# Kernel tuning notes

Hardware: AMD Instinct MI355X
Metric: run time of the kernel (lower is better)

## Reference

```python
import jax, jax.numpy as jnp
import numpy as np

B, S, D_MODEL, H = 2, 2048, 2048, 16
DQK = D_MODEL // H            # 128
DV = D_MODEL * 2 // H // 3    # 85 (GLU branch)
SCALE = DQK ** -0.5
ROPE_BASE = 10000.0


def apply_rope(x):
    # x: [B, S, H, D], NeoX-style half rotation
    D = x.shape[-1]
    half = D // 2
    inv_freq = 1.0 / (ROPE_BASE ** (jnp.arange(half, dtype=jnp.float32) / half))
    ang = jnp.arange(x.shape[1], dtype=jnp.float32)[:, None] * inv_freq[None, :]  # [S, half]
    cos = jnp.cos(ang)[None, :, None, :]
    sin = jnp.sin(ang)[None, :, None, :]
    x1, x2 = x[..., :half], x[..., half:]
    return jnp.concatenate([x1 * cos - x2 * sin, x2 * cos + x1 * sin], axis=-1)


def setup_inputs() -> dict:
    key = jax.random.key(0)
    ks = jax.random.split(key, 12)
    init = lambda k, shape, fan_in: jax.random.uniform(k, shape, jnp.float32, -1.0, 1.0) * (fan_in ** -0.5)
    q = jax.random.normal(ks[0], (B, S, D_MODEL), jnp.float32)
    k = jax.random.normal(ks[1], (B, S, D_MODEL), jnp.float32)
    v = jax.random.normal(ks[2], (B, S, D_MODEL), jnp.float32)
    # causal boolean mask: True = masked (upper triangle)
    mask = jnp.triu(jnp.ones((S, S), dtype=bool), k=1)
    Wq = init(ks[3], (D_MODEL, DQK * H), D_MODEL)
    bq = init(ks[4], (DQK * H,), D_MODEL)
    Wk = init(ks[5], (D_MODEL, DQK * H), D_MODEL)
    bk = init(ks[6], (DQK * H,), D_MODEL)
    Wv = init(ks[7], (D_MODEL, DV * H * 2), D_MODEL)
    bv = init(ks[8], (DV * H * 2,), D_MODEL)
    Wo = init(ks[9], (DV * H, D_MODEL), DV * H)
    bo = init(ks[10], (D_MODEL,), DV * H)
    return {"q": q, "k": k, "v": v, "mask": mask,
            "Wq": Wq, "bq": bq, "Wk": Wk, "bk": bk,
            "Wv": Wv, "bv": bv, "Wo": Wo, "bo": bo}


def reference(q, k, v, mask, Wq, bq, Wk, bk, Wv, bv, Wo, bo):
    qp = q @ Wq + bq                      # [B,S,H*DQK]
    kp = k @ Wk + bk                      # [B,S,H*DQK]
    vp = v @ Wv + bv                      # [B,S,2*H*DV]
    # GLU over the FULL last dim (matches torch chunk(2, dim=-1) before unflatten)
    half = DV * H
    vg = vp[..., :half] * jax.nn.silu(vp[..., half:])   # [B,S,H*DV]
    qh = qp.reshape(B, S, H, DQK)
    kh = kp.reshape(B, S, H, DQK)
    vh = vg.reshape(B, S, H, DV)
    qh = apply_rope(qh)
    kh = apply_rope(kh)
    # [B,H,S,D]
    qh = qh.transpose(0, 2, 1, 3)
    kh = kh.transpose(0, 2, 1, 3)
    vh = vh.transpose(0, 2, 1, 3)
    score = jnp.einsum('bhqd,bhkd->bhqk', qh, kh) * SCALE  # [B,H,S,S]
    score = jnp.where(mask[None, None, :, :], -jnp.inf, score)
    attn = jax.nn.softmax(score, axis=-1)
    o = jnp.einsum('bhqk,bhkd->bhqd', attn, vh)            # [B,H,S,DV]
    o = o.transpose(0, 2, 1, 3).reshape(B, S, H * DV)
    return o @ Wo + bo                                     # [B,S,D_MODEL]
```

## Files before the change

### kernel.cpp

```cpp
#include <hip/hip_runtime.h>
#include <cstdint>
#include <cmath>

typedef __bf16 bf16;
typedef __bf16 bf16x8 __attribute__((ext_vector_type(8)));
typedef float f32x4 __attribute__((ext_vector_type(4)));

#define B_      2
#define S_      2048
#define H_      16
#define DQK_    128
#define DV_     85
#define DVP_    96
#define DMODEL_ 2048
#define NKV_    1360
#define KH_     1536
#define NV_     2720
#define NVP_    2816
#define SCALE_  0.08838834764831845f
#define QSCALE_ 0.12752044442215615f
#define M2_     16.0f
#define L2_10K_ 13.287712379549449f

__device__ __forceinline__ void lds_cp16(const void* g, void* l) {
    __builtin_amdgcn_global_load_lds(
        (const __attribute__((address_space(1))) unsigned int*)(uintptr_t)g,
        (__attribute__((address_space(3))) unsigned int*)(uintptr_t)l,
        16, 0, 0);
}

__global__ __launch_bounds__(256) void detect_dtype(const unsigned int* __restrict__ w,
                                                    int* __restrict__ flag) {
    __shared__ int cnt;
    if (threadIdx.x == 0) cnt = 0;
    __syncthreads();
    unsigned v = w[threadIdx.x];
    unsigned e = (v >> 7) & 0xFFu;
    if (e > 100u && e < 140u) atomicAdd(&cnt, 1);
    __syncthreads();
    if (threadIdx.x == 0) *flag = (cnt >= 200) ? 1 : 0;
}

__global__ __launch_bounds__(256) void norm_mat(const void* __restrict__ src, bf16* __restrict__ dst,
                                                const int* __restrict__ flag, long n8) {
    long i = (long)blockIdx.x * 256 + threadIdx.x;
    if (i >= n8) return;
    if (*flag) {
        ((bf16x8*)dst)[i] = ((const bf16x8*)src)[i];
    } else {
        const float* s = (const float*)src;
        bf16x8 v;
#pragma unroll
        for (int j = 0; j < 8; ++j) v[j] = (bf16)s[i * 8 + j];
        ((bf16x8*)dst)[i] = v;
    }
}

__global__ __launch_bounds__(256) void norm_bias4(
    const void* __restrict__ s0, const void* __restrict__ s1,
    const void* __restrict__ s2, const void* __restrict__ s3,
    float* __restrict__ d0, float* __restrict__ d1,
    float* __restrict__ d2, float* __restrict__ d3,
    const int* __restrict__ flag) {
    int j = blockIdx.x * 256 + threadIdx.x;
    const void* s; float* d;
    if (j < DMODEL_) { s = s0; d = d0; }
    else if ((j -= DMODEL_) < DMODEL_) { s = s1; d = d1; }
    else if ((j -= DMODEL_) < NV_) { s = s2; d = d2; }
    else if ((j -= NV_) < DMODEL_) { s = s3; d = d3; }
    else return;
    d[j] = (*flag) ? (float)((const bf16*)s)[j] : ((const float*)s)[j];
}

__global__ __launch_bounds__(256) void transpose_qk_dyn(
    const void* __restrict__ inq, const void* __restrict__ ink,
    bf16* __restrict__ outq, bf16* __restrict__ outk, const int* __restrict__ flag) {
    __shared__ bf16 tile[32][33];
    const bool isbf = (*flag != 0);
    const void* in = blockIdx.z ? ink : inq;
    bf16* out = blockIdx.z ? outk : outq;
    int r0 = blockIdx.x * 32, c0 = blockIdx.y * 32;
    int tx = threadIdx.x, ty = threadIdx.y;
#pragma unroll
    for (int i = 0; i < 32; i += 8) {
        size_t idx = (size_t)(r0 + ty + i) * DMODEL_ + c0 + tx;
        tile[ty + i][tx] = isbf ? ((const bf16*)in)[idx] : (bf16)((const float*)in)[idx];
    }
    __syncthreads();
#pragma unroll
    for (int i = 0; i < 32; i += 8)
        out[(size_t)(c0 + ty + i) * DMODEL_ + r0 + tx] = tile[tx][ty + i];
}

__global__ __launch_bounds__(256) void transpose_wvi_dyn(
    const void* __restrict__ in, bf16* __restrict__ out, const int* __restrict__ flag) {
    __shared__ bf16 tile[32][34];
    const bool isbf = (*flag != 0);
    int n0 = blockIdx.x * 32, k0 = blockIdx.y * 32;
    int tx = threadIdx.x, ty = threadIdx.y;
    int fl = (n0 >> 1) + (tx & 15), vg = tx >> 4;
    int c = vg * NKV_ + fl;
    int nl = 2 * (tx & 15) + vg;
#pragma unroll
    for (int i = 0; i < 32; i += 8) {
        bf16 v = (bf16)0.0f;
        if (fl < NKV_) {
            size_t idx = (size_t)(k0 + ty + i) * NV_ + c;
            v = isbf ? ((const bf16*)in)[idx] : (bf16)((const float*)in)[idx];
        }
        tile[ty + i][nl] = v;
    }
    __syncthreads();
#pragma unroll
    for (int i = 0; i < 32; i += 8)
        out[(size_t)(n0 + ty + i) * DMODEL_ + k0 + tx] = tile[tx][ty + i];
}

__global__ __launch_bounds__(256) void transpose_wo_dyn(
    const void* __restrict__ in, bf16* __restrict__ out, const int* __restrict__ flag) {
    __shared__ bf16 tile[32][33];
    const bool isbf = (*flag != 0);
    int k0 = blockIdx.x * 32, n0 = blockIdx.y * 32;
    int tx = threadIdx.x, ty = threadIdx.y;
#pragma unroll
    for (int i = 0; i < 32; i += 8) {
        int k = k0 + ty + i, c = n0 + tx;
        int hh = k / DVP_, dd = k - hh * DVP_;
        bf16 v = (bf16)0.0f;
        if (dd < DV_) {
            size_t idx = (size_t)(hh * DV_ + dd) * DMODEL_ + c;
            v = isbf ? ((const bf16*)in)[idx] : (bf16)((const float*)in)[idx];
        }
        tile[ty + i][tx] = v;
    }
    __syncthreads();
#pragma unroll
    for (int i = 0; i < 32; i += 8) {
        int n = n0 + ty + i, k = k0 + tx;
        out[(size_t)n * KH_ + k] = tile[tx][ty + i];
    }
}

template <int NT, class AF>
__device__ __forceinline__ void gemm256_loop(
    AF aaddr, const bf16* __restrict__ Bt, int ldb, int n0,
    bf16* sA, bf16* sB, f32x4 (&acc)[8][4])
{
    const int tid = threadIdx.x, lane = tid & 63, w = tid >> 6;
    const int fm = lane & 15, quad = lane >> 4;
    const int wm = (w >> 2) * 128, wn = (w & 3) * 64;
    const int row0 = tid >> 2;
    const int kk8 = (((tid >> 3) ^ tid) & 3) * 8;
    const int qsz = (quad ^ ((fm >> 1) & 3)) * 8;

    auto stageA = [&](int u) {
        const int ri = u & 3, c = u * 32 + kk8;
        lds_cp16(aaddr(row0, c),       &sA[ri * 8192 + w * 512]);
        lds_cp16(aaddr(row0 + 128, c), &sA[ri * 8192 + 4096 + w * 512]);
    };
    auto stageB = [&](int u) {
        const int ri = u & 3, c = u * 32 + kk8;
        lds_cp16(Bt + (size_t)(n0 + row0) * ldb + c,       &sB[ri * 8192 + w * 512]);
        lds_cp16(Bt + (size_t)(n0 + row0 + 128) * ldb + c, &sB[ri * 8192 + 4096 + w * 512]);
    };

    stageA(0); stageB(0); stageA(1); stageB(1);
    asm volatile("s_waitcnt vmcnt(4)" ::: "memory");
    __builtin_amdgcn_sched_barrier(0);
    __builtin_amdgcn_s_barrier();
    __builtin_amdgcn_sched_barrier(0);

    for (int t = 0; t < NT; ++t) {
        const int u0 = 2 * t;
        const bool pre = (t + 1 < NT);
        bf16x8 af[8], bfv[2];
#pragma unroll
        for (int p = 0; p < 4; ++p) {
            const int kh = p >> 1, nh = p & 1;
            const int ri = (u0 + kh) & 3;
            if (nh == 0) {
#pragma unroll
                for (int i = 0; i < 8; ++i)
                    af[i] = *(const bf16x8*)&sA[ri * 8192 + (wm + i * 16 + fm) * 32 + qsz];
            }
#pragma unroll
            for (int j = 0; j < 2; ++j)
                bfv[j] = *(const bf16x8*)&sB[ri * 8192 + (wn + nh * 32 + j * 16 + fm) * 32 + qsz];
            if (pre) {
                if      (p == 0) stageA(u0 + 2);
                else if (p == 1) stageB(u0 + 2);
                else if (p == 2) stageA(u0 + 3);
                else             stageB(u0 + 3);
            }
            __builtin_amdgcn_sched_barrier(0);
            __builtin_amdgcn_s_barrier();
            asm volatile("s_waitcnt lgkmcnt(0)" ::: "memory");
            __builtin_amdgcn_sched_barrier(0);
            __builtin_amdgcn_s_setprio(1);
#pragma unroll
            for (int i = 0; i < 8; ++i)
#pragma unroll
                for (int j = 0; j < 2; ++j)
                    acc[i][nh * 2 + j] = __builtin_amdgcn_mfma_f32_16x16x32_bf16(
                        af[i], bfv[j], acc[i][nh * 2 + j], 0, 0, 0);
            __builtin_amdgcn_s_setprio(0);
            __builtin_amdgcn_sched_barrier(0);
            if (nh == 1) {
                if (pre) asm volatile("s_waitcnt vmcnt(4)" ::: "memory");
                else     asm volatile("s_waitcnt vmcnt(0)" ::: "memory");
                __builtin_amdgcn_sched_barrier(0);
            }
            __builtin_amdgcn_s_barrier();
            __builtin_amdgcn_sched_barrier(0);
        }
    }
}

__global__ __launch_bounds__(512, 2) void gemm_qk_rope256(
    const bf16* __restrict__ Aq, const bf16* __restrict__ Ak,
    const bf16* __restrict__ Btq, const bf16* __restrict__ Btk,
    const float* __restrict__ bq, const float* __restrict__ bk,
    bf16* __restrict__ qt, bf16* __restrict__ ktp) {
    extern __shared__ char smem[];
    bf16* sA = (bf16*)smem;
    bf16* sB = (bf16*)(smem + 65536);
    const int z = blockIdx.z;
    const bf16* A     = z ? Ak  : Aq;
    const bf16* Bt    = z ? Btk : Btq;
    const float* bias = z ? bk  : bq;
    bf16* dst         = z ? ktp : qt;
    const float qs    = z ? 1.0f : QSCALE_;
    const int tid = threadIdx.x, lane = tid & 63, w = tid >> 6;
    const int fm = lane & 15, quad = lane >> 4;
    const int wm = (w >> 2) * 128, wn = (w & 3) * 64;
    const int m0 = blockIdx.x * 256, n0 = blockIdx.y * 256;
    f32x4 acc[8][4] = {};
    auto aaddr = [&](int row, int k) -> const bf16* {
        return A + (size_t)(m0 + row) * DMODEL_ + k;
    };
    gemm256_loop<32>(aaddr, Bt, DMODEL_, n0, sA, sB, acc);

    float bv[4];
#pragma unroll
    for (int jn = 0; jn < 4; ++jn) bv[jn] = bias[n0 + wn + jn * 16 + fm];
    const int b = m0 >> 11, sb = m0 & (S_ - 1);
    const int hbase = n0 >> 7;
    bf16* ep = (bf16*)smem;
    __syncthreads();
#pragma unroll
    for (int g = 0; g < 4; ++g) {
        if ((w >> 2) == (g >> 1)) {
#pragma unroll
            for (int i2 = 0; i2 < 4; ++i2) {
                const int i = (g & 1) * 4 + i2;
#pragma unroll
                for (int jn = 0; jn < 4; ++jn)
#pragma unroll
                    for (int r = 0; r < 4; ++r)
                        ep[(i2 * 16 + quad * 4 + r) * 264 + wn + jn * 16 + fm] =
                            (bf16)(acc[i][jn][r] + bv[jn]);
            }
        }
        __syncthreads();
#pragma unroll
        for (int it2 = 0; it2 < 4; ++it2) {
            int task = it2 * 512 + tid;
            int lr = task >> 5, ch = task & 31;
            int s = sb + g * 64 + lr;
            int h = hbase + (ch >> 4);
            int cl0 = (ch * 8) & 127;
            bf16x8 v  = *(const bf16x8*)&ep[lr * 264 + ch * 8];
            bf16x8 uu = *(const bf16x8*)&ep[lr * 264 + ((ch * 8) ^ 64)];
            bf16x8 o8;
#pragma unroll
            for (int j = 0; j < 8; ++j) {
                int cl = cl0 + j, dd = cl & 63;
                float ang = (float)s * exp2f(-(float)dd * (L2_10K_ / 64.0f));
                float sn, cs;
                __sincosf(ang, &sn, &cs);
                float x = (float)v[j], y = (float)uu[j];
                float ov = (cl < 64) ? (x * cs - y * sn) : (x * cs + y * sn);
                o8[j] = (bf16)(ov * qs);
            }
            *(bf16x8*)&dst[((size_t)(b * H_ + h) * S_ + s) * DQK_ + cl0] = o8;
        }
        __syncthreads();
    }
}

__global__ __launch_bounds__(512, 2) void gemm_v_swiglu256(
    const bf16* __restrict__ A, const bf16* __restrict__ Bt,
    const float* __restrict__ bias, bf16* __restrict__ vt) {
    extern __shared__ char smem[];
    bf16* sA = (bf16*)smem;
    bf16* sB = (bf16*)(smem + 65536);
    const int tid = threadIdx.x, lane = tid & 63, w = tid >> 6;
    const int fm = lane & 15, quad = lane >> 4;
    const int wm = (w >> 2) * 128, wn = (w & 3) * 64;
    const int m0 = blockIdx.x * 256, n0 = blockIdx.y * 256;
    f32x4 acc[8][4] = {};
    auto aaddr = [&](int row, int k) -> const bf16* {
        return A + (size_t)(m0 + row) * DMODEL_ + k;
    };
    gemm256_loop<32>(aaddr, Bt, DMODEL_, n0, sA, sB, acc);

    float bv[4];
#pragma unroll
    for (int jn = 0; jn < 4; ++jn) {
        int col = n0 + wn + jn * 16 + fm;
        bv[jn] = (col < NV_) ? bias[(col & 1) * NKV_ + (col >> 1)] : 0.0f;
    }
    bf16* ep2 = (bf16*)smem;
    __syncthreads();
    const bool isval = ((fm & 1) == 0);
    const int flb = (wn >> 1) + (fm >> 1);
#pragma unroll
    for (int i = 0; i < 8; ++i)
#pragma unroll
        for (int jn = 0; jn < 4; ++jn)
#pragma unroll
            for (int r = 0; r < 4; ++r) {
                float ag = acc[i][jn][r] + bv[jn];
                float part = __shfl_xor(ag, 1, 64);
                if (isval) {
                    float gg = part;
                    float out = ag * gg / (1.0f + __expf(-gg));
                    ep2[(flb + jn * 8) * 264 + wm + i * 16 + quad * 4 + r] = (bf16)out;
                }
            }
    __syncthreads();
    const int b = m0 >> 11, s0 = m0 & (S_ - 1);
#pragma unroll
    for (int it2 = 0; it2 < 8; ++it2) {
        int task = it2 * 512 + tid;
        int fl_local = task >> 5, ch = task & 31;
        int flat = blockIdx.y * 128 + fl_local;
        if (flat < NKV_) {
            int h = (flat * 1543) >> 17;
            int d = flat - h * DV_;
            bf16x8 vv = *(const bf16x8*)&ep2[fl_local * 264 + ch * 8];
            *(bf16x8*)&vt[((size_t)(b * H_ + h) * DVP_ + d) * S_ + s0 + ch * 8] = vv;
        }
    }
}

__global__ __launch_bounds__(256) void vt_pad(bf16* __restrict__ vt) {
    int idx = blockIdx.x * 256 + threadIdx.x;
    if (idx >= 32 * 11 * 2048) return;
    int s = idx & (S_ - 1);
    int rest = idx >> 11;
    int dpad = 85 + rest % 11;
    int bh = rest / 11;
    vt[((size_t)bh * DVP_ + dpad) * S_ + s] = (bf16)((dpad == 95) ? 1.0f : 0.0f);
}

__global__ __launch_bounds__(256) void gemm_bt_oh(
    const bf16* __restrict__ Oh, const bf16* __restrict__ Bt,
    const float* __restrict__ bias, bf16* __restrict__ C, float* __restrict__ Cf,
    const int* __restrict__ outflag) {
    __shared__ bf16 As[128 * 32];
    __shared__ bf16 Bs[128 * 32];
    const int t = threadIdx.x, lane = t & 63, w = t >> 6;
    const int m0 = blockIdx.x * 128, n0 = blockIdx.y * 128;
    const int wm = (w >> 1) * 64, wn = (w & 1) * 64;
    const int fm = lane & 15, quad = lane >> 4, fk = quad * 8;
    const int srow = lane >> 2, scol = (lane & 3) * 8;
    f32x4 acc[4][4] = {};
    for (int k0 = 0; k0 < KH_; k0 += 32) {
        __syncthreads();
#pragma unroll
        for (int j = 0; j < 2; ++j) {
            int c = j * 4 + w;
            int m = m0 + c * 16 + srow;
            int k = k0 + scol;
            int hh = k / DVP_, dd = k - hh * DVP_;
            const bf16* ga = Oh + ((size_t)((m >> 11) * H_ + hh) * S_ + (m & (S_ - 1))) * DVP_ + dd;
            lds_cp16(ga, &As[c * 512]);
            lds_cp16(Bt + (size_t)(n0 + c * 16 + srow) * KH_ + k0 + scol, &Bs[c * 512]);
        }
        __syncthreads();
        bf16x8 af[4], bfr[4];
#pragma unroll
        for (int i = 0; i < 4; ++i) {
            af[i]  = *(const bf16x8*)&As[(wm + i * 16 + fm) * 32 + fk];
            bfr[i] = *(const bf16x8*)&Bs[(wn + i * 16 + fm) * 32 + fk];
        }
#pragma unroll
        for (int i = 0; i < 4; ++i)
#pragma unroll
            for (int jn = 0; jn < 4; ++jn)
                acc[i][jn] = __builtin_amdgcn_mfma_f32_16x16x32_bf16(af[i], bfr[jn], acc[i][jn], 0, 0, 0);
    }
    bool bf16out = (*outflag != 0);
#pragma unroll
    for (int jn = 0; jn < 4; ++jn) {
        int col = n0 + wn + jn * 16 + fm;
        float bv = bias[col];
#pragma unroll
        for (int i = 0; i < 4; ++i) {
            int rowb = m0 + wm + i * 16 + quad * 4;
            if (bf16out) {
#pragma unroll
                for (int r = 0; r < 4; ++r)
                    C[(size_t)(rowb + r) * DMODEL_ + col] = (bf16)(acc[i][jn][r] + bv);
            } else {
#pragma unroll
                for (int r = 0; r < 4; ++r)
                    Cf[(size_t)(rowb + r) * DMODEL_ + col] = acc[i][jn][r] + bv;
            }
        }
    }
}

__global__ __launch_bounds__(256) void attn_split(
    const bf16* __restrict__ qt, const bf16* __restrict__ kt,
    const bf16* __restrict__ vt,
    bf16* __restrict__ Opart, float* __restrict__ lpart) {
    const int bh = blockIdx.x, qb = blockIdx.y, split = blockIdx.z;
    if (split * 8 > qb) return;
    __shared__ bf16 Ks[64 * 128];
    __shared__ bf16 Vs[96 * 64];
    __shared__ bf16 plds[4][16 * 72];
    const int t = threadIdx.x, lane = t & 63, w = t >> 6;
    const int fm = lane & 15, quad = lane >> 4;
    const int h = bh & 15, b = bh >> 4;
    const int q0 = qb * 64 + w * 16;
    const int g = qb >> 3;
    const int pidx = bh * 80 + 4 * g * (g + 1) + (qb & 7) * (g + 1) + split;

    const bf16* qbase = qt + ((size_t)(b * H_ + h) * S_ + q0 + fm) * DQK_ + quad * 8;
    bf16x8 aq[4];
#pragma unroll
    for (int kb = 0; kb < 4; ++kb) aq[kb] = *(const bf16x8*)(qbase + kb * 32);
    const bf16* kbase = kt + (size_t)(b * H_ + h) * S_ * DQK_;
    const bf16* vbase = vt + (size_t)(b * H_ + h) * DVP_ * S_;

    const float NEG_INF = -__builtin_inff();
    f32x4 oacc[6] = {};
    bf16* pl = &plds[w][0];

    const int t0 = split * 8;
    const int t1 = min(t0 + 8, qb + 1);
    for (int it = t0; it < t1; ++it) {
        const int k0 = it * 64;
        __syncthreads();
#pragma unroll
        for (int iw = 0; iw < 4; ++iw) {
            int flat = (w * 4 + iw) * 64 + lane;
            int r = flat >> 4, c = (flat & 15) ^ (r & 15);
            lds_cp16(kbase + (size_t)(k0 + r) * DQK_ + c * 8, &Ks[(w * 4 + iw) * 512]);
        }
#pragma unroll
        for (int iw = 0; iw < 3; ++iw) {
            int flat = (w * 3 + iw) * 64 + lane;
            int r = flat >> 3, c = (flat & 7) ^ (r & 7);
            lds_cp16(vbase + (size_t)r * S_ + k0 + c * 8, &Vs[(w * 3 + iw) * 512]);
        }
        __syncthreads();
        f32x4 sc[4] = {};
#pragma unroll
        for (int nt = 0; nt < 4; ++nt) {
            if (k0 + nt * 16 <= q0 + 15) {
                const int row16 = (nt * 16 + fm) * 16;
#pragma unroll
                for (int kb = 0; kb < 4; ++kb) {
                    const bf16* kp = &Ks[(row16 + ((kb * 4 + quad) ^ fm)) * 8];
                    sc[nt] = __builtin_amdgcn_mfma_f32_16x16x32_bf16(aq[kb], *(const bf16x8*)kp, sc[nt], 0, 0, 0);
                }
            }
        }
        if (it == qb) {
#pragma unroll
            for (int nt = 0; nt < 4; ++nt) {
                int col = k0 + nt * 16 + fm;
#pragma unroll
                for (int r = 0; r < 4; ++r) {
                    int rowq = q0 + quad * 4 + r;
                    if (col > rowq) sc[nt][r] = NEG_INF;
                }
            }
        }
#pragma unroll
        for (int nt = 0; nt < 4; ++nt)
#pragma unroll
            for (int r = 0; r < 4; ++r)
                pl[(quad * 4 + r) * 72 + nt * 16 + fm] =
                    (bf16)__builtin_amdgcn_exp2f(sc[nt][r] - M2_);
        asm volatile("s_waitcnt lgkmcnt(0)" ::: "memory");
        bf16x8 pa0 = *(const bf16x8*)(pl + fm * 72 + quad * 8);
        bf16x8 pa1 = *(const bf16x8*)(pl + fm * 72 + 32 + quad * 8);
#pragma unroll
        for (int n2 = 0; n2 < 6; ++n2) {
            int row8 = (n2 * 16 + fm) * 8;
            const bf16* v0 = &Vs[(row8 + (quad ^ (fm & 7))) * 8];
            const bf16* v1 = &Vs[(row8 + ((4 + quad) ^ (fm & 7))) * 8];
            oacc[n2] = __builtin_amdgcn_mfma_f32_16x16x32_bf16(pa0, *(const bf16x8*)v0, oacc[n2], 0, 0, 0);
            oacc[n2] = __builtin_amdgcn_mfma_f32_16x16x32_bf16(pa1, *(const bf16x8*)v1, oacc[n2], 0, 0, 0);
        }
    }
    float lv[4], inv_l[4];
#pragma unroll
    for (int r = 0; r < 4; ++r) {
        lv[r] = __shfl(oacc[5][r], (lane & 48) | 15, 64);
        inv_l[r] = (lv[r] > 0.f) ? 1.0f / lv[r] : 0.0f;
    }
    if (fm == 0) {
#pragma unroll
        for (int r = 0; r < 4; ++r) {
            int row = w * 16 + quad * 4 + r;
            lpart[(size_t)pidx * 64 + row] = lv[r];
        }
    }
#pragma unroll
    for (int n2 = 0; n2 < 6; ++n2)
#pragma unroll
        for (int r = 0; r < 4; ++r) {
            int row = w * 16 + quad * 4 + r;
            Opart[((size_t)pidx * 64 + row) * DVP_ + n2 * 16 + fm] = (bf16)(oacc[n2][r] * inv_l[r]);
        }
}

__global__ __launch_bounds__(256) void attn_combine2(
    const bf16* __restrict__ Opart, const float* __restrict__ lpart,
    bf16* __restrict__ oh) {
    const int bh = blockIdx.x, qb = blockIdx.y;
    const int g = qb >> 3, nact = g + 1;
    const int pidx0 = bh * 80 + 4 * g * (g + 1) + (qb & 7) * (g + 1);
    const int t = threadIdx.x;
#pragma unroll
    for (int i = 0; i < 3; ++i) {
        int idx = i * 256 + t;
        int row = idx / 12, ch = idx - row * 12;
        float W = 0.f, wgt[4];
        for (int p = 0; p < nact; ++p) {
            wgt[p] = lpart[(size_t)(pidx0 + p) * 64 + row];
            W += wgt[p];
        }
        float invW = (W > 0.f) ? 1.0f / W : 0.0f;
        float acc[8] = {};
        for (int p = 0; p < nact; ++p) {
            bf16x8 v = *(const bf16x8*)&Opart[((size_t)(pidx0 + p) * 64 + row) * DVP_ + ch * 8];
#pragma unroll
            for (int j = 0; j < 8; ++j) acc[j] += wgt[p] * (float)v[j];
        }
        bf16x8 o8;
#pragma unroll
        for (int j = 0; j < 8; ++j) o8[j] = (bf16)(acc[j] * invW);
        *(bf16x8*)&oh[((size_t)bh * S_ + qb * 64 + row) * DVP_ + ch * 8] = o8;
    }
}

extern "C" void kernel_launch(void* const* d_in, const int* in_sizes, int n_in,
                              void* d_out, int out_size, void* d_ws, size_t ws_size,
                              hipStream_t stream) {
    const void* qin = d_in[0];
    const void* kin = d_in[1];
    const void* vin = d_in[2];
    const void* Wq = d_in[4];
    const void* bq = d_in[5];
    const void* Wk = d_in[6];
    const void* bk = d_in[7];
    const void* Wv = d_in[8];
    const void* bv = d_in[9];
    const void* Wo = d_in[10];
    const void* bo = d_in[11];

    char* ws = (char*)d_ws;
    bf16* qt   = (bf16*)(ws);
    bf16* ktp  = (bf16*)(ws + 16777216);
    char* R1   = ws + 33554432;
    bf16* scrq = (bf16*)(R1);
    bf16* scrk = (bf16*)(R1 + 16777216);
    bf16* wTq  = (bf16*)(R1 + 33554432);
    bf16* wTk  = (bf16*)(R1 + 41943040);
    bf16* scrv = (bf16*)(R1);
    bf16* wTvi = (bf16*)(R1 + 16777216);
    bf16*  wTo   = (bf16*)(R1);
    bf16*  Opart = (bf16*)(R1 + 6291456);
    float* lpart = (float*)(R1 + 37748736);
    bf16* vtp = (bf16*)(ws + 84148224);
    bf16* oh  = (bf16*)(ws + 96731136);
    float* bqf = (float*)(ws + 109314048);
    float* bkf = bqf + DMODEL_;
    float* bvf = bkf + DMODEL_;
    float* bof = bvf + NV_;
    int*  flag = (int*)(bof + DMODEL_);

    dim3 tb(32, 8);
    auto nblk = [](long n8) { return (int)((n8 + 255) / 256); };
    long n8_x = (long)B_ * S_ * DMODEL_ / 8;

    static bool attr_done = false;
    if (!attr_done) {
        hipFuncSetAttribute((const void*)gemm_qk_rope256,
                            hipFuncAttributeMaxDynamicSharedMemorySize, 131072);
        hipFuncSetAttribute((const void*)gemm_v_swiglu256,
                            hipFuncAttributeMaxDynamicSharedMemorySize, 131072);
        attr_done = true;
    }

    detect_dtype<<<1, 256, 0, stream>>>((const unsigned int*)qin, flag);
    norm_bias4<<<(3 * DMODEL_ + NV_ + 255) / 256, 256, 0, stream>>>(
        bq, bk, bv, bo, bqf, bkf, bvf, bof, flag);
    vt_pad<<<(32 * 11 * 2048) / 256, 256, 0, stream>>>(vtp);

    norm_mat<<<nblk(n8_x), 256, 0, stream>>>(qin, scrq, flag, n8_x);
    norm_mat<<<nblk(n8_x), 256, 0, stream>>>(kin, scrk, flag, n8_x);
    transpose_qk_dyn<<<dim3(64, 64, 2), tb, 0, stream>>>(Wq, Wk, wTq, wTk, flag);
    gemm_qk_rope256<<<dim3(16, 8, 2), 512, 131072, stream>>>(
        scrq, scrk, wTq, wTk, bqf, bkf, qt, ktp);

    norm_mat<<<nblk(n8_x), 256, 0, stream>>>(vin, scrv, flag, n8_x);
    transpose_wvi_dyn<<<dim3(NVP_ / 32, DMODEL_ / 32), tb, 0, stream>>>(Wv, wTvi, flag);
    gemm_v_swiglu256<<<dim3(16, NVP_ / 256), 512, 131072, stream>>>(scrv, wTvi, bvf, vtp);

    transpose_wo_dyn<<<dim3(KH_ / 32, DMODEL_ / 32), tb, 0, stream>>>(Wo, wTo, flag);

    attn_split<<<dim3(32, 32, 4), 256, 0, stream>>>(qt, ktp, vtp, Opart, lpart);
    attn_combine2<<<dim3(32, 32), 256, 0, stream>>>(Opart, lpart, oh);

    gemm_bt_oh<<<dim3(32, 16), 256, 0, stream>>>(oh, wTo, bof, (bf16*)d_out, (float*)d_out, flag);
}
```

Measured before the change: 486.3 us.

## Deepen A-operand prefetch to three stages in 256x256 GEMM loop

Reworks the shared GEMM main loop so the A tiles use a three-deep LDS ring (six slots) and B tiles a two-deep ring, prefetching A two iterations ahead. Each sub-step now splits the work by M-half and covers both K halves, instead of splitting by K-half. The aim is to hide global-load latency behind more MFMA work. It raises dynamic LDS from 128KB to 160KB per block for the QK and V projection GEMMs, which likely drops residency from two blocks per CU to one.

```diff
diff --git a/kernel.cpp b/kernel.cpp
--- a/kernel.cpp
+++ b/kernel.cpp
@@ -153,18 +153,20 @@
     const int kk8 = (((tid >> 3) ^ tid) & 3) * 8;
     const int qsz = (quad ^ ((fm >> 1) & 3)) * 8;
 
-    auto stageA = [&](int u) {
-        const int ri = u & 3, c = u * 32 + kk8;
-        lds_cp16(aaddr(row0, c),       &sA[ri * 8192 + w * 512]);
-        lds_cp16(aaddr(row0 + 128, c), &sA[ri * 8192 + 4096 + w * 512]);
+    auto stageA = [&](int u, int sl) {
+        const int c = u * 32 + kk8;
+        lds_cp16(aaddr(row0, c),       &sA[sl * 8192 + w * 512]);
+        lds_cp16(aaddr(row0 + 128, c), &sA[sl * 8192 + 4096 + w * 512]);
     };
-    auto stageB = [&](int u) {
-        const int ri = u & 3, c = u * 32 + kk8;
-        lds_cp16(Bt + (size_t)(n0 + row0) * ldb + c,       &sB[ri * 8192 + w * 512]);
-        lds_cp16(Bt + (size_t)(n0 + row0 + 128) * ldb + c, &sB[ri * 8192 + 4096 + w * 512]);
+    auto stageB = [&](int u, int sl) {
+        const int c = u * 32 + kk8;
+        lds_cp16(Bt + (size_t)(n0 + row0) * ldb + c,       &sB[sl * 8192 + w * 512]);
+        lds_cp16(Bt + (size_t)(n0 + row0 + 128) * ldb + c, &sB[sl * 8192 + 4096 + w * 512]);
     };
 
-    stageA(0); stageB(0); stageA(1); stageB(1);
+    stageA(0, 0); stageA(1, 1);
+    stageB(0, 0); stageB(1, 1);
+    stageA(2, 2); stageA(3, 3);
     asm volatile("s_waitcnt vmcnt(4)" ::: "memory");
     __builtin_amdgcn_sched_barrier(0);
     __builtin_amdgcn_s_barrier();
@@ -172,25 +174,38 @@
 
     for (int t = 0; t < NT; ++t) {
         const int u0 = 2 * t;
-        const bool pre = (t + 1 < NT);
-        bf16x8 af[8], bfv[2];
+        const int tm3 = t % 3;
+        const int slA0 = 2 * tm3;
+        const int slB0 = 2 * (t & 1);
+        const int slAs = 2 * ((t + 2) % 3);
+        const int slBs = 2 * ((t + 1) & 1);
+        const bf16* tA0 = sA + slA0 * 8192;
+        const bf16* tA1 = tA0 + 8192;
+        const bf16* tB0 = sB + slB0 * 8192;
+        const bf16* tB1 = tB0 + 8192;
 #pragma unroll
         for (int p = 0; p < 4; ++p) {
-            const int kh = p >> 1, nh = p & 1;
-            const int ri = (u0 + kh) & 3;
-            if (nh == 0) {
-#pragma unroll
-                for (int i = 0; i < 8; ++i)
-                    af[i] = *(const bf16x8*)&sA[ri * 8192 + (wm + i * 16 + fm) * 32 + qsz];
-            }
-#pragma unroll
-            for (int j = 0; j < 2; ++j)
-                bfv[j] = *(const bf16x8*)&sB[ri * 8192 + (wn + nh * 32 + j * 16 + fm) * 32 + qsz];
-            if (pre) {
-                if      (p == 0) stageA(u0 + 2);
-                else if (p == 1) stageB(u0 + 2);
-                else if (p == 2) stageA(u0 + 3);
-                else             stageB(u0 + 3);
+            const int mh = p >> 1, nh = p & 1;
+            bf16x8 af[2][4], bfv[2][2];
+#pragma unroll
+            for (int i = 0; i < 4; ++i) {
+                const int ro = (wm + mh * 64 + i * 16 + fm) * 32 + qsz;
+                af[0][i] = *(const bf16x8*)&tA0[ro];
+                af[1][i] = *(const bf16x8*)&tA1[ro];
+            }
+#pragma unroll
+            for (int j = 0; j < 2; ++j) {
+                const int ro = (wn + nh * 32 + j * 16 + fm) * 32 + qsz;
+                bfv[0][j] = *(const bf16x8*)&tB0[ro];
+                bfv[1][j] = *(const bf16x8*)&tB1[ro];
+            }
+            if (t + 1 < NT) {
+                if      (p == 0) stageB(u0 + 2, slBs);
+                else if (p == 1) stageB(u0 + 3, slBs + 1);
+                else if (t + 2 < NT) {
+                    if (p == 2) stageA(u0 + 4, slAs);
+                    else        stageA(u0 + 5, slAs + 1);
+                }
             }
             __builtin_amdgcn_sched_barrier(0);
             __builtin_amdgcn_s_barrier();
@@ -198,16 +213,18 @@
             __builtin_amdgcn_sched_barrier(0);
             __builtin_amdgcn_s_setprio(1);
 #pragma unroll
-            for (int i = 0; i < 8; ++i)
-#pragma unroll
-                for (int j = 0; j < 2; ++j)
-                    acc[i][nh * 2 + j] = __builtin_amdgcn_mfma_f32_16x16x32_bf16(
-                        af[i], bfv[j], acc[i][nh * 2 + j], 0, 0, 0);
+            for (int kh = 0; kh < 2; ++kh)
+#pragma unroll
+                for (int i = 0; i < 4; ++i)
+#pragma unroll
+                    for (int j = 0; j < 2; ++j)
+                        acc[mh * 4 + i][nh * 2 + j] = __builtin_amdgcn_mfma_f32_16x16x32_bf16(
+                            af[kh][i], bfv[kh][j], acc[mh * 4 + i][nh * 2 + j], 0, 0, 0);
             __builtin_amdgcn_s_setprio(0);
             __builtin_amdgcn_sched_barrier(0);
-            if (nh == 1) {
-                if (pre) asm volatile("s_waitcnt vmcnt(4)" ::: "memory");
-                else     asm volatile("s_waitcnt vmcnt(0)" ::: "memory");
+            if (p == 3) {
+                if      (t + 2 < NT) asm volatile("s_waitcnt vmcnt(4)" ::: "memory");
+                else if (t + 1 < NT) asm volatile("s_waitcnt vmcnt(0)" ::: "memory");
                 __builtin_amdgcn_sched_barrier(0);
             }
             __builtin_amdgcn_s_barrier();
@@ -223,7 +240,7 @@
     bf16* __restrict__ qt, bf16* __restrict__ ktp) {
     extern __shared__ char smem[];
     bf16* sA = (bf16*)smem;
-    bf16* sB = (bf16*)(smem + 65536);
+    bf16* sB = (bf16*)(smem + 98304);
     const int z = blockIdx.z;
     const bf16* A     = z ? Ak  : Aq;
     const bf16* Bt    = z ? Btk : Btq;
@@ -293,7 +310,7 @@
     const float* __restrict__ bias, bf16* __restrict__ vt) {
     extern __shared__ char smem[];
     bf16* sA = (bf16*)smem;
-    bf16* sB = (bf16*)(smem + 65536);
+    bf16* sB = (bf16*)(smem + 98304);
     const int tid = threadIdx.x, lane = tid & 63, w = tid >> 6;
     const int fm = lane & 15, quad = lane >> 4;
     const int wm = (w >> 2) * 128, wn = (w & 3) * 64;
@@ -593,9 +610,9 @@
     static bool attr_done = false;
     if (!attr_done) {
         hipFuncSetAttribute((const void*)gemm_qk_rope256,
-                            hipFuncAttributeMaxDynamicSharedMemorySize, 131072);
+                            hipFuncAttributeMaxDynamicSharedMemorySize, 163840);
         hipFuncSetAttribute((const void*)gemm_v_swiglu256,
-                            hipFuncAttributeMaxDynamicSharedMemorySize, 131072);
+                            hipFuncAttributeMaxDynamicSharedMemorySize, 163840);
         attr_done = true;
     }
 
@@ -607,12 +624,12 @@
     norm_mat<<<nblk(n8_x), 256, 0, stream>>>(qin, scrq, flag, n8_x);
     norm_mat<<<nblk(n8_x), 256, 0, stream>>>(kin, scrk, flag, n8_x);
     transpose_qk_dyn<<<dim3(64, 64, 2), tb, 0, stream>>>(Wq, Wk, wTq, wTk, flag);
-    gemm_qk_rope256<<<dim3(16, 8, 2), 512, 131072, stream>>>(
+    gemm_qk_rope256<<<dim3(16, 8, 2), 512, 163840, stream>>>(
         scrq, scrk, wTq, wTk, bqf, bkf, qt, ktp);
 
     norm_mat<<<nblk(n8_x), 256, 0, stream>>>(vin, scrv, flag, n8_x);
     transpose_wvi_dyn<<<dim3(NVP_ / 32, DMODEL_ / 32), tb, 0, stream>>>(Wv, wTvi, flag);
-    gemm_v_swiglu256<<<dim3(16, NVP_ / 256), 512, 131072, stream>>>(scrv, wTvi, bvf, vtp);
+    gemm_v_swiglu256<<<dim3(16, NVP_ / 256), 512, 163840, stream>>>(scrv, wTvi, bvf, vtp);
 
     transpose_wo_dyn<<<dim3(KH_ / 32, DMODEL_ / 32), tb, 0, stream>>>(Wo, wTo, flag);
 
```

Measured after the change: 500.8 us. 1.03x slower.
